# Optimization experiments

Measured on AMD Instinct MI355X. Metric: run time of the kernel, lower is better.

The kernel has to match this reference:

```python
import jax, jax.numpy as jnp
import numpy as np
import math

B, SQ, SK, D = 16, 2048, 2048, 64


def setup_inputs() -> dict:
    key = jax.random.key(0)
    kq, kk, kv, kl = jax.random.split(key, 4)
    queries = jax.random.normal(kq, (B, SQ, D), dtype=jnp.float32)
    keys = jax.random.normal(kk, (B, SK, D), dtype=jnp.float32)
    values = jax.random.normal(kv, (B, SK, D), dtype=jnp.float32)
    # valid key lengths in [1, SK]
    valid_lens = jax.random.randint(kl, (B,), 1, SK + 1, dtype=jnp.int32)
    return {"queries": queries, "keys": keys, "values": values, "valid_lens": valid_lens}


def reference(queries, keys, values, valid_lens):
    d = queries.shape[-1]
    # [B, SQ, SK] raw scores
    scores = jnp.einsum("bqd,bkd->bqk", queries, keys) / math.sqrt(d)
    # masked_softmax: key positions >= valid_len are set to -1e6 (d2l semantics)
    kpos = jnp.arange(scores.shape[-1], dtype=jnp.int32)  # [SK]
    mask = kpos[None, None, :] < valid_lens[:, None, None]  # [B,1,SK] -> broadcast
    scores = jnp.where(mask, scores, jnp.float32(-1e6))
    attn = jax.nn.softmax(scores, axis=-1)
    # dropout rate is 0.0 -> identity
    return jnp.einsum("bqk,bkd->bqd", attn, values)
```

## Files before the change

kernel.cpp:

```cpp
#include <hip/hip_runtime.h>

#define NB 16
#define SQL 2048
#define SKL 2048
#define DH 64
#define NSPLIT 8
#define CHUNK 256

typedef __attribute__((ext_vector_type(8)))  short bf16x8;
typedef __attribute__((ext_vector_type(4)))  unsigned short u16x4;
typedef __attribute__((ext_vector_type(8)))  unsigned short u16x8;
typedef __attribute__((ext_vector_type(4)))  float f32x4;
typedef __attribute__((ext_vector_type(16))) float f32x16;

#define LOG2E 1.4426950408889634f
#define K1 (0.125f * LOG2E)

__device__ __forceinline__ unsigned short f2bf(float f) {
    unsigned int u = __builtin_bit_cast(unsigned int, f);
    u += 0x7fffu + ((u >> 16) & 1u);
    return (unsigned short)(u >> 16);
}
__device__ __forceinline__ float bf2f(unsigned short h) {
    return __builtin_bit_cast(float, (unsigned int)h << 16);
}
__device__ __forceinline__ bf16x8 pack8(float4 a, float4 b) {
    u16x8 o;
    o[0] = f2bf(a.x); o[1] = f2bf(a.y); o[2] = f2bf(a.z); o[3] = f2bf(a.w);
    o[4] = f2bf(b.x); o[5] = f2bf(b.y); o[6] = f2bf(b.z); o[7] = f2bf(b.w);
    return __builtin_bit_cast(bf16x8, o);
}

__global__ __launch_bounds__(256) void prep_kernel(
    const float* __restrict__ V, unsigned short* __restrict__ Vt) {
    const int t  = blockIdx.x;
    const int b  = t >> 5;
    const int kb = (t & 31) << 6;
    __shared__ float tile[64][65];
    const int tid = threadIdx.x;
    {
        const int r  = tid >> 2;
        const int cg = (tid & 3) << 4;
        const float* vsrc = V + ((size_t)b * SKL + (kb + r)) * DH;
        #pragma unroll
        for (int i = 0; i < 4; ++i) {
            float4 x = *(const float4*)(vsrc + cg + i * 4);
            tile[r][cg + i*4 + 0] = x.x;
            tile[r][cg + i*4 + 1] = x.y;
            tile[r][cg + i*4 + 2] = x.z;
            tile[r][cg + i*4 + 3] = x.w;
        }
    }
    __syncthreads();
    {
        const int d  = tid >> 2;
        const int kg = (tid & 3) << 4;
        unsigned short* dst = Vt + ((size_t)b * DH + d) * SKL + kb + kg;
        u16x8 o0, o1;
        #pragma unroll
        for (int j = 0; j < 8; ++j) o0[j] = f2bf(tile[kg + j][d]);
        #pragma unroll
        for (int j = 0; j < 8; ++j) o1[j] = f2bf(tile[kg + 8 + j][d]);
        *(u16x8*)(dst)     = o0;
        *(u16x8*)(dst + 8) = o1;
    }
}

__global__ __launch_bounds__(256, 3) void attn_kernel(
    const float* __restrict__ Q,
    const float* __restrict__ K,
    const unsigned short* __restrict__ Vt,
    const int* __restrict__ valid_lens,
    unsigned short* __restrict__ Opart,
    float2* __restrict__ MLpart,
    float* __restrict__ out) {
    const int qblk  = blockIdx.x;
    const int split = blockIdx.y;
    const int b     = blockIdx.z;

    const int valid  = valid_lens[b];
    const int kstart = split * CHUNK;
    if (kstart >= valid) return;
    const int kend    = (valid < kstart + CHUNK) ? valid : (kstart + CHUNK);
    const int ntiles  = (kend - kstart + 63) >> 6;
    const int nactive = (valid + CHUNK - 1) / CHUNK;

    const int tid  = threadIdx.x;
    const int wave = tid >> 6;
    const int lane = tid & 63;
    const int l31  = lane & 31;
    const int h2   = lane >> 5;
    const int sw   = l31 & 7;

    __shared__ unsigned short Klds[64][64];
    __shared__ unsigned short Vlds[64][64];
    __shared__ unsigned short Plds[4][32][64];

    const int q0 = qblk * 128 + wave * 32;
    const float* qptr = Q + ((size_t)b * SQL + q0 + l31) * DH + h2 * 8;
    bf16x8 qf[4];
    #pragma unroll
    for (int ks = 0; ks < 4; ++ks)
        qf[ks] = pack8(*(const float4*)(qptr + ks * 16),
                       *(const float4*)(qptr + ks * 16 + 4));

    const float* kbase = K + (size_t)b * SKL * DH;
    const unsigned short* vbase = Vt + (size_t)b * DH * SKL;

    f32x16 o[2];
    #pragma unroll
    for (int i = 0; i < 2; ++i)
        #pragma unroll
        for (int r = 0; r < 16; ++r) o[i][r] = 0.f;
    float mrow = -1e30f, lrow = 0.f;

    float4 kra[2], krb[2];
    u16x8  vreg[2];
    #pragma unroll
    for (int i = 0; i < 2; ++i) {
        const int c = i * 256 + tid, r = c >> 3, col = (c & 7) << 3;
        kra[i]  = *(const float4*)(kbase + (size_t)(kstart + r) * DH + col);
        krb[i]  = *(const float4*)(kbase + (size_t)(kstart + r) * DH + col + 4);
        vreg[i] = *(const u16x8*)(vbase + (size_t)r * SKL + kstart + col);
    }

    for (int kt = 0; kt < ntiles; ++kt) {
        const int kb = kstart + (kt << 6);
        __syncthreads();
        #pragma unroll
        for (int i = 0; i < 2; ++i) {
            const int c = i * 256 + tid, r = c >> 3;
            const int pc = ((c & 7) ^ (r & 7)) << 3;
            *(bf16x8*)&Klds[r][pc] = pack8(kra[i], krb[i]);
            *(u16x8*)&Vlds[r][pc]  = vreg[i];
        }
        __syncthreads();
        if (kt + 1 < ntiles) {
            const int kn = kb + 64;
            #pragma unroll
            for (int i = 0; i < 2; ++i) {
                const int c = i * 256 + tid, r = c >> 3, col = (c & 7) << 3;
                kra[i]  = *(const float4*)(kbase + (size_t)(kn + r) * DH + col);
                krb[i]  = *(const float4*)(kbase + (size_t)(kn + r) * DH + col + 4);
                vreg[i] = *(const u16x8*)(vbase + (size_t)r * SKL + kn + col);
            }
        }

        f32x16 s[2];
        #pragma unroll
        for (int t = 0; t < 2; ++t) {
            #pragma unroll
            for (int r = 0; r < 16; ++r) s[t][r] = 0.f;
            #pragma unroll
            for (int ks = 0; ks < 4; ++ks) {
                const bf16x8 kf = *(const bf16x8*)
                    &Klds[t * 32 + l31][((2 * ks + h2) ^ sw) << 3];
                s[t] = __builtin_amdgcn_mfma_f32_32x32x16_bf16(kf, qf[ks], s[t], 0, 0, 0);
            }
        }

        if (kb + 64 > kend) {
            #pragma unroll
            for (int t = 0; t < 2; ++t)
                #pragma unroll
                for (int r = 0; r < 16; ++r)
                    if (kb + t * 32 + (r & 3) + 8 * (r >> 2) + 4 * h2 >= kend)
                        s[t][r] = -1e30f;
        }

        float tmax = -1e30f;
        #pragma unroll
        for (int t = 0; t < 2; ++t)
            #pragma unroll
            for (int r = 0; r < 16; ++r) tmax = fmaxf(tmax, s[t][r]);
        tmax = fmaxf(tmax, __shfl_xor(tmax, 32));

        const float mnew  = fmaxf(mrow, 0.125f * tmax);
        const float alpha = exp2f((mrow - mnew) * LOG2E);
        const float mk    = mnew * LOG2E;
        float rs = 0.f;
        #pragma unroll
        for (int t = 0; t < 2; ++t)
            #pragma unroll
            for (int r = 0; r < 16; ++r) {
                const float p = exp2f(fmaf(s[t][r], K1, -mk));
                s[t][r] = p;
                rs += p;
            }
        rs += __shfl_xor(rs, 32);
        lrow = lrow * alpha + rs;
        mrow = mnew;
        #pragma unroll
        for (int i = 0; i < 2; ++i)
            #pragma unroll
            for (int r = 0; r < 16; ++r) o[i][r] *= alpha;

        #pragma unroll
        for (int t = 0; t < 2; ++t)
            #pragma unroll
            for (int g = 0; g < 4; ++g) {
                u16x4 pw;
                pw[0] = f2bf(s[t][g * 4 + 0]); pw[1] = f2bf(s[t][g * 4 + 1]);
                pw[2] = f2bf(s[t][g * 4 + 2]); pw[3] = f2bf(s[t][g * 4 + 3]);
                const int unit = (4 * t + g) ^ sw;
                *(u16x4*)&Plds[wave][l31][(unit << 3) + (h2 << 2)] = pw;
            }
        bf16x8 pf[4];
        #pragma unroll
        for (int ks = 0; ks < 4; ++ks)
            pf[ks] = *(const bf16x8*)&Plds[wave][l31][((2 * ks + h2) ^ sw) << 3];

        #pragma unroll
        for (int dt = 0; dt < 2; ++dt)
            #pragma unroll
            for (int ks = 0; ks < 4; ++ks) {
                const bf16x8 vf = *(const bf16x8*)
                    &Vlds[dt * 32 + l31][((2 * ks + h2) ^ sw) << 3];
                o[dt] = __builtin_amdgcn_mfma_f32_32x32x16_bf16(vf, pf[ks], o[dt], 0, 0, 0);
            }
    }

    if (nactive == 1) {
        const float inv = 1.0f / lrow;
        float* op = out + ((size_t)b * SQL + q0 + l31) * DH;
        #pragma unroll
        for (int dt = 0; dt < 2; ++dt)
            #pragma unroll
            for (int g = 0; g < 4; ++g) {
                f32x4 ov;
                ov[0] = o[dt][g*4+0] * inv; ov[1] = o[dt][g*4+1] * inv;
                ov[2] = o[dt][g*4+2] * inv; ov[3] = o[dt][g*4+3] * inv;
                *(f32x4*)(op + dt * 32 + 8 * g + 4 * h2) = ov;
            }
        return;
    }

    unsigned short* op = Opart +
        (((size_t)b * NSPLIT + split) * SQL + q0 + l31) * DH;
    #pragma unroll
    for (int dt = 0; dt < 2; ++dt)
        #pragma unroll
        for (int g = 0; g < 4; ++g) {
            u16x4 ow;
            ow[0] = f2bf(o[dt][g * 4 + 0]); ow[1] = f2bf(o[dt][g * 4 + 1]);
            ow[2] = f2bf(o[dt][g * 4 + 2]); ow[3] = f2bf(o[dt][g * 4 + 3]);
            *(u16x4*)(op + dt * 32 + 8 * g + 4 * h2) = ow;
        }
    if (h2 == 0)
        MLpart[((size_t)b * NSPLIT + split) * SQL + q0 + l31] =
            make_float2(mrow, lrow);
}

__global__ __launch_bounds__(256) void reduce_kernel(
    const unsigned short* __restrict__ Opart, const float2* __restrict__ MLpart,
    const int* __restrict__ valid_lens, float* __restrict__ out) {
    const int b   = blockIdx.y;
    const int ns  = (valid_lens[b] + CHUNK - 1) / CHUNK;
    if (ns == 1) return;
    const int tid = threadIdx.x;
    const int q   = blockIdx.x * 64 + (tid >> 2);
    const int dg  = (tid & 3) << 4;

    float m[NSPLIT], l[NSPLIT];
    float M = -1e30f;
    for (int s = 0; s < ns; ++s) {
        float2 ml = MLpart[((size_t)b * NSPLIT + s) * SQL + q];
        m[s] = ml.x; l[s] = ml.y;
        M = fmaxf(M, ml.x);
    }
    float L = 0.f;
    float acc[16];
    #pragma unroll
    for (int i = 0; i < 16; ++i) acc[i] = 0.f;
    for (int s = 0; s < ns; ++s) {
        const float w = exp2f((m[s] - M) * LOG2E);
        L += l[s] * w;
        const unsigned short* p =
            Opart + (((size_t)b * NSPLIT + s) * SQL + q) * DH + dg;
        u16x8 a0 = *(const u16x8*)(p);
        u16x8 a1 = *(const u16x8*)(p + 8);
        #pragma unroll
        for (int i = 0; i < 8; ++i) acc[i]     += w * bf2f(a0[i]);
        #pragma unroll
        for (int i = 0; i < 8; ++i) acc[8 + i] += w * bf2f(a1[i]);
    }
    const float inv = 1.0f / L;
    float* op = out + ((size_t)b * SQL + q) * DH + dg;
    f32x4 ov;
    #pragma unroll
    for (int i = 0; i < 4; ++i) {
        ov[0] = acc[i*4+0] * inv; ov[1] = acc[i*4+1] * inv;
        ov[2] = acc[i*4+2] * inv; ov[3] = acc[i*4+3] * inv;
        *(f32x4*)(op + i * 4) = ov;
    }
}

extern "C" void kernel_launch(void* const* d_in, const int* in_sizes, int n_in,
                              void* d_out, int out_size, void* d_ws, size_t ws_size,
                              hipStream_t stream) {
    const float* Q  = (const float*)d_in[0];
    const float* K  = (const float*)d_in[1];
    const float* V  = (const float*)d_in[2];
    const int*   vl = (const int*)d_in[3];
    float* out = (float*)d_out;

    unsigned short* Vt = (unsigned short*)d_ws;
    unsigned short* Opart = Vt + (size_t)NB * SKL * DH;
    float2* MLpart = (float2*)(Opart + (size_t)NB * NSPLIT * SQL * DH);

    prep_kernel<<<dim3(512), dim3(256), 0, stream>>>(V, Vt);
    attn_kernel<<<dim3(SQL / 128, NSPLIT, NB), dim3(256), 0, stream>>>(
        Q, K, Vt, vl, Opart, MLpart, out);
    reduce_kernel<<<dim3(SQL / 64, NB), dim3(256), 0, stream>>>(
        Opart, MLpart, vl, out);
}
```

Baseline: 111.1 us.

## Double-buffer K/V in LDS, shuffle P in registers, skip unneeded rescales

Keeps two LDS buffers for the K and V tiles so each iteration needs one barrier instead of two. The per-wave P staging buffer in LDS is replaced by cross-half-wave shuffles that build the bf16 P fragments directly in registers. Rescaling of the output accumulator is skipped when no row max grew in the wave. Occupancy is raised to 4 blocks per CU, which adds register pressure and may cause spills.

```diff
diff --git a/kernel.cpp b/kernel.cpp
--- a/kernel.cpp
+++ b/kernel.cpp
@@ -10,6 +10,7 @@
 typedef __attribute__((ext_vector_type(8)))  short bf16x8;
 typedef __attribute__((ext_vector_type(4)))  unsigned short u16x4;
 typedef __attribute__((ext_vector_type(8)))  unsigned short u16x8;
+typedef __attribute__((ext_vector_type(4)))  unsigned int   u32x4;
 typedef __attribute__((ext_vector_type(4)))  float f32x4;
 typedef __attribute__((ext_vector_type(16))) float f32x16;
 
@@ -29,6 +30,9 @@
     o[0] = f2bf(a.x); o[1] = f2bf(a.y); o[2] = f2bf(a.z); o[3] = f2bf(a.w);
     o[4] = f2bf(b.x); o[5] = f2bf(b.y); o[6] = f2bf(b.z); o[7] = f2bf(b.w);
     return __builtin_bit_cast(bf16x8, o);
+}
+__device__ __forceinline__ unsigned int pack2(float a, float b) {
+    return (unsigned int)f2bf(a) | ((unsigned int)f2bf(b) << 16);
 }
 
 __global__ __launch_bounds__(256) void prep_kernel(
@@ -66,7 +70,7 @@
     }
 }
 
-__global__ __launch_bounds__(256, 3) void attn_kernel(
+__global__ __launch_bounds__(256, 4) void attn_kernel(
     const float* __restrict__ Q,
     const float* __restrict__ K,
     const unsigned short* __restrict__ Vt,
@@ -86,17 +90,15 @@
     const int nactive = (valid + CHUNK - 1) / CHUNK;
 
     const int tid  = threadIdx.x;
-    const int wave = tid >> 6;
     const int lane = tid & 63;
     const int l31  = lane & 31;
     const int h2   = lane >> 5;
     const int sw   = l31 & 7;
 
-    __shared__ unsigned short Klds[64][64];
-    __shared__ unsigned short Vlds[64][64];
-    __shared__ unsigned short Plds[4][32][64];
-
-    const int q0 = qblk * 128 + wave * 32;
+    __shared__ unsigned short Klds[2][64][64];
+    __shared__ unsigned short Vlds[2][64][64];
+
+    const int q0 = qblk * 128 + (tid >> 6) * 32;
     const float* qptr = Q + ((size_t)b * SQL + q0 + l31) * DH + h2 * 8;
     bf16x8 qf[4];
     #pragma unroll
@@ -116,35 +118,37 @@
 
     float4 kra[2], krb[2];
     u16x8  vreg[2];
+    const int src_r   = tid >> 3;
+    const int src_col = (tid & 7) << 3;
     #pragma unroll
     for (int i = 0; i < 2; ++i) {
-        const int c = i * 256 + tid, r = c >> 3, col = (c & 7) << 3;
-        kra[i]  = *(const float4*)(kbase + (size_t)(kstart + r) * DH + col);
-        krb[i]  = *(const float4*)(kbase + (size_t)(kstart + r) * DH + col + 4);
-        vreg[i] = *(const u16x8*)(vbase + (size_t)r * SKL + kstart + col);
+        const int r = src_r + i * 32;
+        kra[i]  = *(const float4*)(kbase + (size_t)(kstart + r) * DH + src_col);
+        krb[i]  = *(const float4*)(kbase + (size_t)(kstart + r) * DH + src_col + 4);
+        vreg[i] = *(const u16x8*)(vbase + (size_t)r * SKL + kstart + src_col);
     }
 
     for (int kt = 0; kt < ntiles; ++kt) {
-        const int kb = kstart + (kt << 6);
-        __syncthreads();
+        const int kb  = kstart + (kt << 6);
+        const int cur = kt & 1;
         #pragma unroll
         for (int i = 0; i < 2; ++i) {
-            const int c = i * 256 + tid, r = c >> 3;
-            const int pc = ((c & 7) ^ (r & 7)) << 3;
-            *(bf16x8*)&Klds[r][pc] = pack8(kra[i], krb[i]);
-            *(u16x8*)&Vlds[r][pc]  = vreg[i];
-        }
-        __syncthreads();
+            const int r  = src_r + i * 32;
+            const int pc = (((tid & 7) ^ (r & 7)) << 3);
+            *(bf16x8*)&Klds[cur][r][pc] = pack8(kra[i], krb[i]);
+            *(u16x8*)&Vlds[cur][r][pc]  = vreg[i];
+        }
         if (kt + 1 < ntiles) {
             const int kn = kb + 64;
             #pragma unroll
             for (int i = 0; i < 2; ++i) {
-                const int c = i * 256 + tid, r = c >> 3, col = (c & 7) << 3;
-                kra[i]  = *(const float4*)(kbase + (size_t)(kn + r) * DH + col);
-                krb[i]  = *(const float4*)(kbase + (size_t)(kn + r) * DH + col + 4);
-                vreg[i] = *(const u16x8*)(vbase + (size_t)r * SKL + kn + col);
-            }
-        }
+                const int r = src_r + i * 32;
+                kra[i]  = *(const float4*)(kbase + (size_t)(kn + r) * DH + src_col);
+                krb[i]  = *(const float4*)(kbase + (size_t)(kn + r) * DH + src_col + 4);
+                vreg[i] = *(const u16x8*)(vbase + (size_t)r * SKL + kn + src_col);
+            }
+        }
+        __syncthreads();
 
         f32x16 s[2];
         #pragma unroll
@@ -154,7 +158,7 @@
             #pragma unroll
             for (int ks = 0; ks < 4; ++ks) {
                 const bf16x8 kf = *(const bf16x8*)
-                    &Klds[t * 32 + l31][((2 * ks + h2) ^ sw) << 3];
+                    &Klds[cur][t * 32 + l31][((2 * ks + h2) ^ sw) << 3];
                 s[t] = __builtin_amdgcn_mfma_f32_32x32x16_bf16(kf, qf[ks], s[t], 0, 0, 0);
             }
         }
@@ -175,9 +179,16 @@
             for (int r = 0; r < 16; ++r) tmax = fmaxf(tmax, s[t][r]);
         tmax = fmaxf(tmax, __shfl_xor(tmax, 32));
 
-        const float mnew  = fmaxf(mrow, 0.125f * tmax);
-        const float alpha = exp2f((mrow - mnew) * LOG2E);
-        const float mk    = mnew * LOG2E;
+        const float mnew = fmaxf(mrow, 0.125f * tmax);
+        float alpha = 1.f;
+        if (__ballot(mnew > mrow)) {
+            alpha = exp2f((mrow - mnew) * LOG2E);
+            #pragma unroll
+            for (int i = 0; i < 2; ++i)
+                #pragma unroll
+                for (int r = 0; r < 16; ++r) o[i][r] *= alpha;
+        }
+        const float mk = mnew * LOG2E;
         float rs = 0.f;
         #pragma unroll
         for (int t = 0; t < 2; ++t)
@@ -190,32 +201,37 @@
         rs += __shfl_xor(rs, 32);
         lrow = lrow * alpha + rs;
         mrow = mnew;
-        #pragma unroll
-        for (int i = 0; i < 2; ++i)
-            #pragma unroll
-            for (int r = 0; r < 16; ++r) o[i][r] *= alpha;
-
+
+        unsigned int pgl[2][4], pgh[2][4];
         #pragma unroll
         for (int t = 0; t < 2; ++t)
             #pragma unroll
             for (int g = 0; g < 4; ++g) {
-                u16x4 pw;
-                pw[0] = f2bf(s[t][g * 4 + 0]); pw[1] = f2bf(s[t][g * 4 + 1]);
-                pw[2] = f2bf(s[t][g * 4 + 2]); pw[3] = f2bf(s[t][g * 4 + 3]);
-                const int unit = (4 * t + g) ^ sw;
-                *(u16x4*)&Plds[wave][l31][(unit << 3) + (h2 << 2)] = pw;
+                pgl[t][g] = pack2(s[t][g * 4 + 0], s[t][g * 4 + 1]);
+                pgh[t][g] = pack2(s[t][g * 4 + 2], s[t][g * 4 + 3]);
             }
         bf16x8 pf[4];
         #pragma unroll
-        for (int ks = 0; ks < 4; ++ks)
-            pf[ks] = *(const bf16x8*)&Plds[wave][l31][((2 * ks + h2) ^ sw) << 3];
+        for (int ks = 0; ks < 4; ++ks) {
+            const int t = ks >> 1, e = ks & 1;
+            const unsigned int kl = h2 ? pgl[t][2*e+1] : pgl[t][2*e];
+            const unsigned int kh = h2 ? pgh[t][2*e+1] : pgh[t][2*e];
+            const unsigned int sl = h2 ? pgl[t][2*e]   : pgl[t][2*e+1];
+            const unsigned int sh = h2 ? pgh[t][2*e]   : pgh[t][2*e+1];
+            const unsigned int rl = __shfl_xor(sl, 32);
+            const unsigned int rh = __shfl_xor(sh, 32);
+            u32x4 fd;
+            fd[0] = h2 ? rl : kl;  fd[1] = h2 ? rh : kh;
+            fd[2] = h2 ? kl : rl;  fd[3] = h2 ? kh : rh;
+            pf[ks] = __builtin_bit_cast(bf16x8, fd);
+        }
 
         #pragma unroll
         for (int dt = 0; dt < 2; ++dt)
             #pragma unroll
             for (int ks = 0; ks < 4; ++ks) {
                 const bf16x8 vf = *(const bf16x8*)
-                    &Vlds[dt * 32 + l31][((2 * ks + h2) ^ sw) << 3];
+                    &Vlds[cur][dt * 32 + l31][((2 * ks + h2) ^ sw) << 3];
                 o[dt] = __builtin_amdgcn_mfma_f32_32x32x16_bf16(vf, pf[ks], o[dt], 0, 0, 0);
             }
     }
```

Result: no change. 112.7 us (+1.4%).
